# Kernel tuning notes

Measured on AMD Instinct MI355X. Metric: run time of the kernel, lower is better.

The kernel has to match this reference:

```python
import jax, jax.numpy as jnp
import numpy as np

N_NODES = 500_000
N_EDGES = 16_000_000


def setup_inputs() -> dict:
    key = jax.random.key(0)
    ks = jax.random.split(key, 10)
    x = jax.random.normal(ks[0], (N_NODES, 8), dtype=jnp.float32)
    edge_index = jax.random.randint(ks[1], (2, N_EDGES), 0, N_NODES, dtype=jnp.int64)
    W1_l = jax.random.normal(ks[2], (8, 32), dtype=jnp.float32) * 0.1
    W1_r = jax.random.normal(ks[3], (8, 32), dtype=jnp.float32) * 0.1
    b1 = jax.random.normal(ks[4], (32,), dtype=jnp.float32) * 0.1
    W2_l = jax.random.normal(ks[5], (32, 16), dtype=jnp.float32) * 0.1
    W2_r = jax.random.normal(ks[6], (32, 16), dtype=jnp.float32) * 0.1
    b2 = jax.random.normal(ks[7], (16,), dtype=jnp.float32) * 0.1
    W_out = jax.random.normal(ks[8], (16, 1), dtype=jnp.float32) * 0.1
    b_out = jax.random.normal(ks[9], (1,), dtype=jnp.float32) * 0.1
    return {"x": x, "edge_index": edge_index, "W1_l": W1_l, "W1_r": W1_r, "b1": b1,
            "W2_l": W2_l, "W2_r": W2_r, "b2": b2, "W_out": W_out, "b_out": b_out}


def _sage_conv(x, src, dst, deg_inv, W_l, W_r, b):
    # mean-aggregate neighbor features: gather x[src], scatter-add to dst, divide by degree
    agg = jax.ops.segment_sum(x[src], dst, num_segments=N_NODES)  # [N, d_in]
    mean_nb = agg * deg_inv[:, None]
    return mean_nb @ W_l + x @ W_r + b


def reference(x, edge_index, W1_l, W1_r, b1, W2_l, W2_r, b2, W_out, b_out):
    src, dst = edge_index[0], edge_index[1]
    # in-degree per target node (mean aggregation denominator), clamped at 1
    deg = jax.ops.segment_sum(jnp.ones((src.shape[0],), dtype=x.dtype), dst,
                              num_segments=N_NODES)
    deg_inv = 1.0 / jnp.maximum(deg, 1.0)
    h = jax.nn.relu(_sage_conv(x, src, dst, deg_inv, W1_l, W1_r, b1))
    # dropout(p=0.1) is identity at inference
    h = jax.nn.relu(_sage_conv(h, src, dst, deg_inv, W2_l, W2_r, b2))
    return jax.nn.sigmoid(h @ W_out + b_out)  # [N, 1]
```

## Files before the change

kernel.cpp:

```cpp
#include <hip/hip_runtime.h>
#include <hip/hip_fp16.h>
#include <math.h>

#define N_NODES 500000
#define N_EDGES 16000000

#define NBUCKET 2048
#define NPB 256
#define NSB 64
#define NSLICE 32
#define NB_USED 1954
#define BUCKET_CAP 9216

#define NCH_H 500
#define CHUNK_H 32000
#define NCH_A 1000
#define CHUNK_A 16000

#define OFF_TOT     0
#define OFF_BASE    8192
#define OFF_FCUR    16512
#define OFF_SBCUR   24704
#define OFF_AUXB    24960
#define OFF_ROW     25600
#define OFF_DEG     2025600
#define OFF_XH8     4025600
#define OFF_PAIRS   8025664
#define OFF_AUX     72025664
#define OFF_H1P8    72025664
#define OFF_S2      80025664
#define OFF_DEGQ    96025664

typedef float v2f __attribute__((ext_vector_type(2)));
typedef unsigned int v4u __attribute__((ext_vector_type(4)));

static __device__ inline float2 up2(unsigned int u) {
  __half2 h = *reinterpret_cast<__half2*>(&u);
  return __half22float2(h);
}
static __device__ inline unsigned int ph2(float a, float b) {
  __half2 h = __floats2half2_rn(a, b);
  return *reinterpret_cast<unsigned int*>(&h);
}
static __device__ inline unsigned int pk_fp8x4(float a, float b, float c, float d) {
  int u = __builtin_amdgcn_cvt_pk_fp8_f32(a, b, 0, false);
  u = __builtin_amdgcn_cvt_pk_fp8_f32(c, d, u, true);
  return (unsigned int)u;
}
static __device__ inline void acc8(float* a, uint2 g) {
  v2f f01 = __builtin_amdgcn_cvt_pk_f32_fp8((int)g.x, false);
  v2f f23 = __builtin_amdgcn_cvt_pk_f32_fp8((int)g.x, true);
  v2f f45 = __builtin_amdgcn_cvt_pk_f32_fp8((int)g.y, false);
  v2f f67 = __builtin_amdgcn_cvt_pk_f32_fp8((int)g.y, true);
  a[0] += f01.x; a[1] += f01.y; a[2] += f23.x; a[3] += f23.y;
  a[4] += f45.x; a[5] += f45.y; a[6] += f67.x; a[7] += f67.y;
}
static __device__ inline void acc16(float* a, uint4 g) {
  v2f f0 = __builtin_amdgcn_cvt_pk_f32_fp8((int)g.x, false);
  v2f f1 = __builtin_amdgcn_cvt_pk_f32_fp8((int)g.x, true);
  v2f f2 = __builtin_amdgcn_cvt_pk_f32_fp8((int)g.y, false);
  v2f f3 = __builtin_amdgcn_cvt_pk_f32_fp8((int)g.y, true);
  v2f f4 = __builtin_amdgcn_cvt_pk_f32_fp8((int)g.z, false);
  v2f f5 = __builtin_amdgcn_cvt_pk_f32_fp8((int)g.z, true);
  v2f f6 = __builtin_amdgcn_cvt_pk_f32_fp8((int)g.w, false);
  v2f f7 = __builtin_amdgcn_cvt_pk_f32_fp8((int)g.w, true);
  a[0] += f0.x;  a[1] += f0.y;  a[2] += f1.x;  a[3] += f1.y;
  a[4] += f2.x;  a[5] += f2.y;  a[6] += f3.x;  a[7] += f3.y;
  a[8] += f4.x;  a[9] += f4.y;  a[10] += f5.x; a[11] += f5.y;
  a[12] += f6.x; a[13] += f6.y; a[14] += f7.x; a[15] += f7.y;
}

__global__ __launch_bounds__(256) void k_xcast(const float* __restrict__ x,
                                               uint2* __restrict__ xh8) {
  int i = blockIdx.x * 256 + threadIdx.x;
  if (i >= N_NODES) return;
  const float4* xp = (const float4*)(x + (size_t)i * 8);
  float4 a = xp[0], b = xp[1];
  uint2 v;
  v.x = pk_fp8x4(a.x, a.y, a.z, a.w);
  v.y = pk_fp8x4(b.x, b.y, b.z, b.w);
  xh8[i] = v;
}

__global__ __launch_bounds__(256) void k_hist(const int* __restrict__ ei,
                                              int* __restrict__ tot) {
  __shared__ int hist[NBUCKET];
  int t = threadIdx.x;
  int c = blockIdx.x;
#pragma unroll
  for (int j = 0; j < NBUCKET / 256; j++) hist[t + j * 256] = 0;
  __syncthreads();
  int e0 = c * CHUNK_H;
  const int ng = CHUNK_H / 4;
  for (int g = t; g < ng; g += 256) {
    uint4 d4 = *(const uint4*)(ei + N_EDGES + e0 + g * 4);
    atomicAdd(&hist[d4.x >> 8], 1);
    atomicAdd(&hist[d4.y >> 8], 1);
    atomicAdd(&hist[d4.z >> 8], 1);
    atomicAdd(&hist[d4.w >> 8], 1);
  }
  __syncthreads();
#pragma unroll
  for (int j = 0; j < NBUCKET / 256; j++) {
    int b = t + j * 256;
    if (hist[b]) atomicAdd(&tot[b], hist[b]);
  }
}

__global__ __launch_bounds__(256) void k_scan(const int* __restrict__ tot,
                                              int* __restrict__ base,
                                              int* __restrict__ fineCur,
                                              int* __restrict__ sbCur,
                                              int* __restrict__ auxBase) {
  __shared__ int lds[256];
  int t = threadIdx.x;
  int loc[8];
  int s = 0;
#pragma unroll
  for (int j = 0; j < 8; j++) {
    loc[j] = s;
    s += tot[t * 8 + j];
  }
  lds[t] = s;
  __syncthreads();
  for (int off = 1; off < 256; off <<= 1) {
    int v = (t >= off) ? lds[t - off] : 0;
    __syncthreads();
    lds[t] += v;
    __syncthreads();
  }
  int eb = (t > 0) ? lds[t - 1] : 0;
#pragma unroll
  for (int j = 0; j < 8; j++) {
    int idx = t * 8 + j;
    int v = eb + loc[j];
    base[idx] = v;
    fineCur[idx] = v;
  }
  if (t == 255) base[NBUCKET] = lds[255];
  if (t < NSB) {
    int v = (t > 0) ? lds[t * 4 - 1] : 0;
    if (t >= 32) v -= lds[127];
    sbCur[t] = v;
    auxBase[t] = v;
  }
}

__global__ __launch_bounds__(256) void k_passA(const int* __restrict__ ei,
                                               int* __restrict__ sbCur,
                                               unsigned int* __restrict__ aux,
                                               int half) {
  __shared__ int hist[NSB];
  __shared__ int cur[NSB];
  int t = threadIdx.x;
  int c = blockIdx.x;
  if (t < NSB) hist[t] = 0;
  __syncthreads();
  int e0 = c * CHUNK_A;
  const int ng = CHUNK_A / 4;
  for (int g = t; g < ng; g += 256) {
    uint4 d4 = *(const uint4*)(ei + N_EDGES + e0 + g * 4);
    unsigned int dd[4] = {d4.x, d4.y, d4.z, d4.w};
#pragma unroll
    for (int j = 0; j < 4; j++) {
      int sb = (int)(dd[j] >> 13);
      if ((sb >> 5) == half) atomicAdd(&hist[sb], 1);
    }
  }
  __syncthreads();
  if (t < NSB) cur[t] = atomicAdd(&sbCur[t], hist[t]);
  __syncthreads();
  for (int g = t; g < ng; g += 256) {
    uint4 s4 = *(const uint4*)(ei + e0 + g * 4);
    uint4 d4 = *(const uint4*)(ei + N_EDGES + e0 + g * 4);
    unsigned int ss[4] = {s4.x, s4.y, s4.z, s4.w};
    unsigned int dd[4] = {d4.x, d4.y, d4.z, d4.w};
#pragma unroll
    for (int j = 0; j < 4; j++) {
      int sb = (int)(dd[j] >> 13);
      if ((sb >> 5) == half) {
        int pos = atomicAdd(&cur[sb], 1);
        aux[pos] = ss[j] | ((dd[j] & 8191u) << 19);
      }
    }
  }
}

__global__ __launch_bounds__(256) void k_passB(const unsigned int* __restrict__ aux,
                                               const int* __restrict__ base,
                                               const int* __restrict__ auxBase,
                                               int* __restrict__ fineCur,
                                               unsigned int* __restrict__ pairs,
                                               int half) {
  __shared__ int hist[32];
  __shared__ int cur[32];
  int t = threadIdx.x;
  int sbl = blockIdx.x / NSLICE;
  int sl = blockIdx.x % NSLICE;
  int sb = half * 32 + sbl;
  int aStart = auxBase[sb];
  int len = base[(sb + 1) << 5] - base[sb << 5];
  int per = (len + NSLICE - 1) / NSLICE;
  int lo = sl * per;
  int hi = lo + per;
  if (hi > len) hi = len;
  if (t < 32) hist[t] = 0;
  __syncthreads();
  for (int k = lo + t; k < hi; k += 256) {
    unsigned int w = aux[aStart + k];
    atomicAdd(&hist[w >> 27], 1);
  }
  __syncthreads();
  if (t < 32) cur[t] = atomicAdd(&fineCur[(sb << 5) + t], hist[t]);
  __syncthreads();
  for (int k = lo + t; k < hi; k += 256) {
    unsigned int w = aux[aStart + k];
    int pos = atomicAdd(&cur[w >> 27], 1);
    pairs[pos] = w;
  }
}

__global__ __launch_bounds__(256) void k_sort(unsigned int* __restrict__ pairs,
                                              const int* __restrict__ base,
                                              int* __restrict__ row,
                                              int* __restrict__ deg,
                                              unsigned int* __restrict__ degq) {
  __shared__ unsigned int sp[BUCKET_CAP];
  __shared__ int hist[1024];
  __shared__ int cur[1024];
  __shared__ int lds[256];
  int t = threadIdx.x;
  int b = blockIdx.x;
  int e0 = base[b];
  int n = base[b + 1] - e0;
  if (n > BUCKET_CAP) n = BUCKET_CAP;
  for (int k = t; k < n; k += 256) sp[k] = pairs[e0 + k];
#pragma unroll
  for (int j = 0; j < 4; j++) hist[t + j * 256] = 0;
  __syncthreads();
  for (int k = t; k < n; k += 256) {
    unsigned int p = sp[k];
    int key = (int)(((p >> 19) & 255u) << 2) | (int)((p & 0x7FFFFu) >> 17);
    atomicAdd(&hist[key], 1);
  }
  __syncthreads();
  int h0 = hist[4 * t], h1 = hist[4 * t + 1], h2 = hist[4 * t + 2], h3 = hist[4 * t + 3];
  int s = h0 + h1 + h2 + h3;
  lds[t] = s;
  __syncthreads();
  for (int off = 1; off < 256; off <<= 1) {
    int v = (t >= off) ? lds[t - off] : 0;
    __syncthreads();
    lds[t] += v;
    __syncthreads();
  }
  int ebase = (t > 0) ? lds[t - 1] : 0;
  cur[4 * t] = e0 + ebase;
  cur[4 * t + 1] = e0 + ebase + h0;
  cur[4 * t + 2] = e0 + ebase + h0 + h1;
  cur[4 * t + 3] = e0 + ebase + h0 + h1 + h2;
  int i = (b << 8) + t;
  if (i < N_NODES) {
    row[i] = e0 + ebase;
    deg[i] = s;
    degq[i] = (unsigned)h0 | ((unsigned)h1 << 8) | ((unsigned)h2 << 16) |
              ((unsigned)h3 << 24);
  }
  __syncthreads();
  for (int k = t; k < n; k += 256) {
    unsigned int p = sp[k];
    int key = (int)(((p >> 19) & 255u) << 2) | (int)((p & 0x7FFFFu) >> 17);
    int pos = atomicAdd(&cur[key], 1);
    pairs[pos] = p & 0x7FFFFu;
  }
}

__global__ __launch_bounds__(256) void k_l1(
    const unsigned int* __restrict__ adj, const int* __restrict__ row,
    const unsigned int* __restrict__ degq, const uint2* __restrict__ xh8,
    const float* __restrict__ x,
    const float* __restrict__ W1l, const float* __restrict__ W1r,
    const float* __restrict__ b1,
    const float* __restrict__ W2l, const float* __restrict__ W2r,
    v4u* __restrict__ h1p8, v4u* __restrict__ s2) {
  __shared__ float sW1l[256], sW1r[256], sb1[32], sW2l[512], sW2r[512];
  int t = threadIdx.x;
  sW1l[t] = W1l[t];
  sW1r[t] = W1r[t];
  sW2l[t] = W2l[t];  sW2l[t + 256] = W2l[t + 256];
  sW2r[t] = W2r[t];  sW2r[t + 256] = W2r[t + 256];
  if (t < 32) sb1[t] = b1[t];
  __syncthreads();

  int i = blockIdx.x * 256 + t;
  if (i >= N_NODES) return;
  int rs = row[i];
  unsigned dq = degq[i];
  int d = (int)((dq & 255u) + ((dq >> 8) & 255u) + ((dq >> 16) & 255u) + (dq >> 24));

  float acc[8] = {0, 0, 0, 0, 0, 0, 0, 0};
  int off = 0;
#pragma unroll
  for (int q = 0; q < 4; q++) {
    int len = (int)((dq >> (8 * q)) & 255u);
    int js = rs + off;
    int j = 0;
    for (; j + 4 <= len; j += 4) {
      int a0 = (int)__builtin_nontemporal_load(&adj[js + j + 0]);
      int a1 = (int)__builtin_nontemporal_load(&adj[js + j + 1]);
      int a2 = (int)__builtin_nontemporal_load(&adj[js + j + 2]);
      int a3 = (int)__builtin_nontemporal_load(&adj[js + j + 3]);
      uint2 g0 = xh8[a0], g1 = xh8[a1], g2 = xh8[a2], g3 = xh8[a3];
      acc8(acc, g0); acc8(acc, g1); acc8(acc, g2); acc8(acc, g3);
    }
    for (; j < len; j++) {
      uint2 g = xh8[(int)__builtin_nontemporal_load(&adj[js + j])];
      acc8(acc, g);
    }
    off += len;
  }

  float dinv = 1.0f / fmaxf((float)d, 1.0f);
  float m[8];
#pragma unroll
  for (int f = 0; f < 8; f++) m[f] = acc[f] * dinv;
  const float4* xp = (const float4*)(x + (size_t)i * 8);
  float4 x0 = xp[0], x1 = xp[1];
  float xv[8] = {x0.x, x0.y, x0.z, x0.w, x1.x, x1.y, x1.z, x1.w};

  float h[32];
#pragma unroll
  for (int jj = 0; jj < 32; jj++) h[jj] = sb1[jj];
#pragma unroll
  for (int k = 0; k < 8; k++) {
#pragma unroll
    for (int jj = 0; jj < 32; jj++) {
      h[jj] = fmaf(m[k], sW1l[k * 32 + jj], h[jj]);
      h[jj] = fmaf(xv[k], sW1r[k * 32 + jj], h[jj]);
    }
  }
#pragma unroll
  for (int jj = 0; jj < 32; jj++) h[jj] = fmaxf(h[jj], 0.0f);

  float p[16], s[16];
#pragma unroll
  for (int jj = 0; jj < 16; jj++) { p[jj] = 0.0f; s[jj] = 0.0f; }
#pragma unroll
  for (int k = 0; k < 32; k++) {
#pragma unroll
    for (int jj = 0; jj < 16; jj++) {
      p[jj] = fmaf(h[k], sW2l[k * 16 + jj], p[jj]);
      s[jj] = fmaf(h[k], sW2r[k * 16 + jj], s[jj]);
    }
  }
  v4u hv;
  hv.x = pk_fp8x4(p[0], p[1], p[2], p[3]);
  hv.y = pk_fp8x4(p[4], p[5], p[6], p[7]);
  hv.z = pk_fp8x4(p[8], p[9], p[10], p[11]);
  hv.w = pk_fp8x4(p[12], p[13], p[14], p[15]);
  __builtin_nontemporal_store(hv, &h1p8[i]);
  v4u slo, shi;
  slo.x = ph2(s[0], s[1]);   slo.y = ph2(s[2], s[3]);
  slo.z = ph2(s[4], s[5]);   slo.w = ph2(s[6], s[7]);
  shi.x = ph2(s[8], s[9]);   shi.y = ph2(s[10], s[11]);
  shi.z = ph2(s[12], s[13]); shi.w = ph2(s[14], s[15]);
  __builtin_nontemporal_store(slo, &s2[(size_t)i * 2]);
  __builtin_nontemporal_store(shi, &s2[(size_t)i * 2 + 1]);
}

__global__ __launch_bounds__(256) void k_l2(
    const unsigned int* __restrict__ adj, const int* __restrict__ row,
    const unsigned int* __restrict__ degq, const uint4* __restrict__ h1p8,
    const v4u* __restrict__ s2, const float* __restrict__ b2,
    const float* __restrict__ Wout, const float* __restrict__ bout,
    float* __restrict__ out) {
  __shared__ float sb2[16], sWo[16], sbo;
  int t = threadIdx.x;
  if (t < 16) { sb2[t] = b2[t]; sWo[t] = Wout[t]; }
  if (t == 0) sbo = bout[0];
  __syncthreads();

  int i = blockIdx.x * 256 + t;
  if (i >= N_NODES) return;
  int rs = row[i];
  unsigned dq = degq[i];
  int d = (int)((dq & 255u) + ((dq >> 8) & 255u) + ((dq >> 16) & 255u) + (dq >> 24));

  float acc[16];
#pragma unroll
  for (int jj = 0; jj < 16; jj++) acc[jj] = 0.0f;
  int off = 0;
#pragma unroll
  for (int q = 0; q < 4; q++) {
    int len = (int)((dq >> (8 * q)) & 255u);
    int js = rs + off;
    int j = 0;
    for (; j + 4 <= len; j += 4) {
      int a0 = (int)__builtin_nontemporal_load(&adj[js + j + 0]);
      int a1 = (int)__builtin_nontemporal_load(&adj[js + j + 1]);
      int a2 = (int)__builtin_nontemporal_load(&adj[js + j + 2]);
      int a3 = (int)__builtin_nontemporal_load(&adj[js + j + 3]);
      uint4 g0 = h1p8[a0], g1 = h1p8[a1], g2 = h1p8[a2], g3 = h1p8[a3];
      acc16(acc, g0); acc16(acc, g1); acc16(acc, g2); acc16(acc, g3);
    }
    for (; j < len; j++) {
      uint4 g = h1p8[(int)__builtin_nontemporal_load(&adj[js + j])];
      acc16(acc, g);
    }
    off += len;
  }

  float dinv = 1.0f / fmaxf((float)d, 1.0f);
  v4u q0 = __builtin_nontemporal_load(&s2[(size_t)i * 2]);
  v4u q1 = __builtin_nontemporal_load(&s2[(size_t)i * 2 + 1]);
  float2 s0 = up2(q0.x), s1 = up2(q0.y), s2v = up2(q0.z), s3 = up2(q0.w);
  float2 s4 = up2(q1.x), s5 = up2(q1.y), s6 = up2(q1.z), s7 = up2(q1.w);
  float sv[16] = {s0.x, s0.y, s1.x, s1.y, s2v.x, s2v.y, s3.x, s3.y,
                  s4.x, s4.y, s5.x, s5.y, s6.x, s6.y, s7.x, s7.y};
  float o = sbo;
#pragma unroll
  for (int c = 0; c < 16; c++) {
    float h2 = fmaxf(acc[c] * dinv + sv[c] + sb2[c], 0.0f);
    o = fmaf(h2, sWo[c], o);
  }
  out[i] = 1.0f / (1.0f + expf(-o));
}

extern "C" void kernel_launch(void* const* d_in, const int* in_sizes, int n_in,
                              void* d_out, int out_size, void* d_ws, size_t ws_size,
                              hipStream_t stream) {
  const float* x    = (const float*)d_in[0];
  const int*   ei   = (const int*)d_in[1];
  const float* W1l  = (const float*)d_in[2];
  const float* W1r  = (const float*)d_in[3];
  const float* b1   = (const float*)d_in[4];
  const float* W2l  = (const float*)d_in[5];
  const float* W2r  = (const float*)d_in[6];
  const float* b2   = (const float*)d_in[7];
  const float* Wout = (const float*)d_in[8];
  const float* bout = (const float*)d_in[9];
  float* out = (float*)d_out;

  char* ws = (char*)d_ws;
  int* tot     = (int*)(ws + OFF_TOT);
  int* base    = (int*)(ws + OFF_BASE);
  int* fineCur = (int*)(ws + OFF_FCUR);
  int* sbCur   = (int*)(ws + OFF_SBCUR);
  int* auxBase = (int*)(ws + OFF_AUXB);
  int* row     = (int*)(ws + OFF_ROW);
  int* deg     = (int*)(ws + OFF_DEG);
  uint2* xh8   = (uint2*)(ws + OFF_XH8);
  unsigned int* pairs = (unsigned int*)(ws + OFF_PAIRS);
  unsigned int* aux   = (unsigned int*)(ws + OFF_AUX);
  v4u* h1p8    = (v4u*)(ws + OFF_H1P8);
  v4u* s2      = (v4u*)(ws + OFF_S2);
  unsigned int* degq = (unsigned int*)(ws + OFF_DEGQ);

  (void)hipMemsetAsync(tot, 0, NBUCKET * sizeof(int), stream);

  k_xcast<<<NB_USED, 256, 0, stream>>>(x, xh8);
  k_hist<<<NCH_H, 256, 0, stream>>>(ei, tot);
  k_scan<<<1, 256, 0, stream>>>(tot, base, fineCur, sbCur, auxBase);
  k_passA<<<NCH_A, 256, 0, stream>>>(ei, sbCur, aux, 0);
  k_passB<<<32 * NSLICE, 256, 0, stream>>>(aux, base, auxBase, fineCur, pairs, 0);
  k_passA<<<NCH_A, 256, 0, stream>>>(ei, sbCur, aux, 1);
  k_passB<<<32 * NSLICE, 256, 0, stream>>>(aux, base, auxBase, fineCur, pairs, 1);
  k_sort<<<NBUCKET, 256, 0, stream>>>(pairs, base, row, deg, degq);
  k_l1<<<NB_USED, 256, 0, stream>>>(pairs, row, degq, xh8, x, W1l, W1r, b1,
                                    W2l, W2r, h1p8, s2);
  k_l2<<<NB_USED, 256, 0, stream>>>(pairs, row, degq, (const uint4*)h1p8, s2,
                                    b2, Wout, bout, out);
}
```

Measured before the change: 880.8 us.

## Stage radix scatter in LDS per tile for coalesced writes; simplify l1 degree loop

The two scatter passes (passA, passB) now bucket each 4000-element tile in shared memory using per-tile histograms and precomputed global bases. They then write contiguous runs per bucket to global memory with nontemporal stores, where before each element was a scattered direct write. The goal is to cut uncoalesced global write traffic in the multi-pass bucket sort, at the cost of extra LDS traffic, more barriers and a serial per-tile prefix done by one thread. Separately, k_l1 reads the plain degree and loops once over the neighbours instead of four quarter-segments decoded from the packed degq.

```diff
diff --git a/kernel.cpp b/kernel.cpp
--- a/kernel.cpp
+++ b/kernel.cpp
@@ -16,6 +16,8 @@
 #define CHUNK_H 32000
 #define NCH_A 1000
 #define CHUNK_A 16000
+#define T_A 4000
+#define T_B 4000
 
 #define OFF_TOT     0
 #define OFF_BASE    8192
@@ -150,39 +152,76 @@
                                                int* __restrict__ sbCur,
                                                unsigned int* __restrict__ aux,
                                                int half) {
-  __shared__ int hist[NSB];
-  __shared__ int cur[NSB];
+  __shared__ unsigned int ldsW[T_A];
+  __shared__ unsigned char sid[T_A];
+  __shared__ int hist[4 * 32];
+  __shared__ int gbase[4 * 32];
+  __shared__ int loff[32];
+  __shared__ int lcur[32];
+  __shared__ int tot_s;
   int t = threadIdx.x;
   int c = blockIdx.x;
-  if (t < NSB) hist[t] = 0;
-  __syncthreads();
   int e0 = c * CHUNK_A;
-  const int ng = CHUNK_A / 4;
-  for (int g = t; g < ng; g += 256) {
-    uint4 d4 = *(const uint4*)(ei + N_EDGES + e0 + g * 4);
-    unsigned int dd[4] = {d4.x, d4.y, d4.z, d4.w};
-#pragma unroll
-    for (int j = 0; j < 4; j++) {
-      int sb = (int)(dd[j] >> 13);
-      if ((sb >> 5) == half) atomicAdd(&hist[sb], 1);
-    }
-  }
-  __syncthreads();
-  if (t < NSB) cur[t] = atomicAdd(&sbCur[t], hist[t]);
-  __syncthreads();
-  for (int g = t; g < ng; g += 256) {
-    uint4 s4 = *(const uint4*)(ei + e0 + g * 4);
-    uint4 d4 = *(const uint4*)(ei + N_EDGES + e0 + g * 4);
-    unsigned int ss[4] = {s4.x, s4.y, s4.z, s4.w};
-    unsigned int dd[4] = {d4.x, d4.y, d4.z, d4.w};
-#pragma unroll
-    for (int j = 0; j < 4; j++) {
-      int sb = (int)(dd[j] >> 13);
-      if ((sb >> 5) == half) {
-        int pos = atomicAdd(&cur[sb], 1);
-        aux[pos] = ss[j] | ((dd[j] & 8191u) << 19);
+  int sb0 = half * 32;
+  if (t < 128) hist[t] = 0;
+  __syncthreads();
+  {
+    const int ng = CHUNK_A / 4;
+    for (int g = t; g < ng; g += 256) {
+      uint4 d4 = *(const uint4*)(ei + N_EDGES + e0 + g * 4);
+      int tile = g / (T_A / 4);
+      unsigned dd[4] = {d4.x, d4.y, d4.z, d4.w};
+#pragma unroll
+      for (int j = 0; j < 4; j++) {
+        int sb = (int)(dd[j] >> 13);
+        if ((sb >> 5) == half) atomicAdd(&hist[tile * 32 + (sb - sb0)], 1);
       }
     }
+  }
+  __syncthreads();
+  if (t < 32) {
+    int h0 = hist[t], h1 = hist[32 + t], h2 = hist[64 + t], h3 = hist[96 + t];
+    int g = atomicAdd(&sbCur[sb0 + t], h0 + h1 + h2 + h3);
+    gbase[t] = g;
+    gbase[32 + t] = g + h0;
+    gbase[64 + t] = g + h0 + h1;
+    gbase[96 + t] = g + h0 + h1 + h2;
+  }
+  __syncthreads();
+  for (int ti = 0; ti < 4; ti++) {
+    if (t == 0) {
+      int r = 0;
+      for (int s = 0; s < 32; s++) {
+        loff[s] = r; lcur[s] = r; r += hist[ti * 32 + s];
+      }
+      tot_s = r;
+    }
+    __syncthreads();
+    int tb = e0 + ti * T_A;
+    const int ng = T_A / 4;
+    for (int g = t; g < ng; g += 256) {
+      uint4 s4 = *(const uint4*)(ei + tb + g * 4);
+      uint4 d4 = *(const uint4*)(ei + N_EDGES + tb + g * 4);
+      unsigned ss[4] = {s4.x, s4.y, s4.z, s4.w};
+      unsigned dd[4] = {d4.x, d4.y, d4.z, d4.w};
+#pragma unroll
+      for (int j = 0; j < 4; j++) {
+        int sb = (int)(dd[j] >> 13);
+        if ((sb >> 5) == half) {
+          int sl = sb - sb0;
+          int pos = atomicAdd(&lcur[sl], 1);
+          ldsW[pos] = ss[j] | ((dd[j] & 8191u) << 19);
+          sid[pos] = (unsigned char)sl;
+        }
+      }
+    }
+    __syncthreads();
+    int tot = tot_s;
+    for (int k = t; k < tot; k += 256) {
+      int s = sid[k];
+      __builtin_nontemporal_store(ldsW[k], &aux[gbase[ti * 32 + s] + (k - loff[s])]);
+    }
+    __syncthreads();
   }
 }
 
@@ -192,8 +231,13 @@
                                                int* __restrict__ fineCur,
                                                unsigned int* __restrict__ pairs,
                                                int half) {
-  __shared__ int hist[32];
-  __shared__ int cur[32];
+  __shared__ unsigned int ldsW[T_B];
+  __shared__ unsigned char sid[T_B];
+  __shared__ int hist[4 * 32];
+  __shared__ int gbase[4 * 32];
+  __shared__ int loff[32];
+  __shared__ int lcur[32];
+  __shared__ int tot_s;
   int t = threadIdx.x;
   int sbl = blockIdx.x / NSLICE;
   int sl = blockIdx.x % NSLICE;
@@ -204,19 +248,51 @@
   int lo = sl * per;
   int hi = lo + per;
   if (hi > len) hi = len;
-  if (t < 32) hist[t] = 0;
+  if (lo >= hi) return;
+  int nt = (hi - lo + T_B - 1) / T_B;
+  if (t < 128) hist[t] = 0;
   __syncthreads();
   for (int k = lo + t; k < hi; k += 256) {
-    unsigned int w = aux[aStart + k];
-    atomicAdd(&hist[w >> 27], 1);
-  }
-  __syncthreads();
-  if (t < 32) cur[t] = atomicAdd(&fineCur[(sb << 5) + t], hist[t]);
-  __syncthreads();
-  for (int k = lo + t; k < hi; k += 256) {
-    unsigned int w = aux[aStart + k];
-    int pos = atomicAdd(&cur[w >> 27], 1);
-    pairs[pos] = w;
+    unsigned w = aux[aStart + k];
+    int tile = (k - lo) / T_B;
+    atomicAdd(&hist[tile * 32 + (int)(w >> 27)], 1);
+  }
+  __syncthreads();
+  if (t < 32) {
+    int h0 = hist[t], h1 = hist[32 + t], h2 = hist[64 + t], h3 = hist[96 + t];
+    int g = atomicAdd(&fineCur[(sb << 5) + t], h0 + h1 + h2 + h3);
+    gbase[t] = g;
+    gbase[32 + t] = g + h0;
+    gbase[64 + t] = g + h0 + h1;
+    gbase[96 + t] = g + h0 + h1 + h2;
+  }
+  __syncthreads();
+  for (int ti = 0; ti < nt; ti++) {
+    if (t == 0) {
+      int r = 0;
+      for (int s = 0; s < 32; s++) {
+        loff[s] = r; lcur[s] = r; r += hist[ti * 32 + s];
+      }
+      tot_s = r;
+    }
+    __syncthreads();
+    int tl = lo + ti * T_B;
+    int te = tl + T_B;
+    if (te > hi) te = hi;
+    for (int k = tl + t; k < te; k += 256) {
+      unsigned w = aux[aStart + k];
+      int s = (int)(w >> 27);
+      int pos = atomicAdd(&lcur[s], 1);
+      ldsW[pos] = w;
+      sid[pos] = (unsigned char)s;
+    }
+    __syncthreads();
+    int tot = tot_s;
+    for (int k = t; k < tot; k += 256) {
+      int s = sid[k];
+      __builtin_nontemporal_store(ldsW[k], &pairs[gbase[ti * 32 + s] + (k - loff[s])]);
+    }
+    __syncthreads();
   }
 }
 
@@ -277,7 +353,7 @@
 
 __global__ __launch_bounds__(256) void k_l1(
     const unsigned int* __restrict__ adj, const int* __restrict__ row,
-    const unsigned int* __restrict__ degq, const uint2* __restrict__ xh8,
+    const int* __restrict__ deg, const uint2* __restrict__ xh8,
     const float* __restrict__ x,
     const float* __restrict__ W1l, const float* __restrict__ W1r,
     const float* __restrict__ b1,
@@ -295,29 +371,21 @@
   int i = blockIdx.x * 256 + t;
   if (i >= N_NODES) return;
   int rs = row[i];
-  unsigned dq = degq[i];
-  int d = (int)((dq & 255u) + ((dq >> 8) & 255u) + ((dq >> 16) & 255u) + (dq >> 24));
+  int d = deg[i];
 
   float acc[8] = {0, 0, 0, 0, 0, 0, 0, 0};
-  int off = 0;
-#pragma unroll
-  for (int q = 0; q < 4; q++) {
-    int len = (int)((dq >> (8 * q)) & 255u);
-    int js = rs + off;
-    int j = 0;
-    for (; j + 4 <= len; j += 4) {
-      int a0 = (int)__builtin_nontemporal_load(&adj[js + j + 0]);
-      int a1 = (int)__builtin_nontemporal_load(&adj[js + j + 1]);
-      int a2 = (int)__builtin_nontemporal_load(&adj[js + j + 2]);
-      int a3 = (int)__builtin_nontemporal_load(&adj[js + j + 3]);
-      uint2 g0 = xh8[a0], g1 = xh8[a1], g2 = xh8[a2], g3 = xh8[a3];
-      acc8(acc, g0); acc8(acc, g1); acc8(acc, g2); acc8(acc, g3);
-    }
-    for (; j < len; j++) {
-      uint2 g = xh8[(int)__builtin_nontemporal_load(&adj[js + j])];
-      acc8(acc, g);
-    }
-    off += len;
+  int j = 0;
+  for (; j + 4 <= d; j += 4) {
+    int a0 = (int)__builtin_nontemporal_load(&adj[rs + j + 0]);
+    int a1 = (int)__builtin_nontemporal_load(&adj[rs + j + 1]);
+    int a2 = (int)__builtin_nontemporal_load(&adj[rs + j + 2]);
+    int a3 = (int)__builtin_nontemporal_load(&adj[rs + j + 3]);
+    uint2 g0 = xh8[a0], g1 = xh8[a1], g2 = xh8[a2], g3 = xh8[a3];
+    acc8(acc, g0); acc8(acc, g1); acc8(acc, g2); acc8(acc, g3);
+  }
+  for (; j < d; j++) {
+    uint2 g = xh8[(int)__builtin_nontemporal_load(&adj[rs + j])];
+    acc8(acc, g);
   }
 
   float dinv = 1.0f / fmaxf((float)d, 1.0f);
@@ -466,7 +534,7 @@
   k_passA<<<NCH_A, 256, 0, stream>>>(ei, sbCur, aux, 1);
   k_passB<<<32 * NSLICE, 256, 0, stream>>>(aux, base, auxBase, fineCur, pairs, 1);
   k_sort<<<NBUCKET, 256, 0, stream>>>(pairs, base, row, deg, degq);
-  k_l1<<<NB_USED, 256, 0, stream>>>(pairs, row, degq, xh8, x, W1l, W1r, b1,
+  k_l1<<<NB_USED, 256, 0, stream>>>(pairs, row, deg, xh8, x, W1l, W1r, b1,
                                     W2l, W2r, h1p8, s2);
   k_l2<<<NB_USED, 256, 0, stream>>>(pairs, row, degq, (const uint4*)h1p8, s2,
                                     b2, Wout, bout, out);
```

Result: faster. 846.6 us (-3.9%).

## Replace two-level aux scatter with single-pass 2048-bucket scatter

Applied to the files above, without the earlier changes.

Drops the two-half superbucket pass (passA/passB through an aux buffer) in favour of a single scatter kernel that histograms all 2048 fine buckets in LDS and writes directly into the pairs array with nontemporal stores. This removes one full read and write of the 16M-edge intermediate plus four kernel launches, but spreads each block's writes across 2048 destinations instead of 32, so coalescing may suffer. It also simplifies the layer-1 gather loop to one flat loop over the degree, and adds block-wide barriers between quarter passes in layer 2, apparently to keep the threads of a block in lockstep for cache locality.

```diff
diff --git a/kernel.cpp b/kernel.cpp
--- a/kernel.cpp
+++ b/kernel.cpp
@@ -6,27 +6,20 @@
 #define N_EDGES 16000000
 
 #define NBUCKET 2048
-#define NPB 256
-#define NSB 64
-#define NSLICE 32
 #define NB_USED 1954
 #define BUCKET_CAP 9216
 
 #define NCH_H 500
 #define CHUNK_H 32000
-#define NCH_A 1000
-#define CHUNK_A 16000
+#define NCH_S 1000
+#define CHUNK_S 16000
 
 #define OFF_TOT     0
 #define OFF_BASE    8192
 #define OFF_FCUR    16512
-#define OFF_SBCUR   24704
-#define OFF_AUXB    24960
 #define OFF_ROW     25600
-#define OFF_DEG     2025600
 #define OFF_XH8     4025600
 #define OFF_PAIRS   8025664
-#define OFF_AUX     72025664
 #define OFF_H1P8    72025664
 #define OFF_S2      80025664
 #define OFF_DEGQ    96025664
@@ -109,9 +102,7 @@
 
 __global__ __launch_bounds__(256) void k_scan(const int* __restrict__ tot,
                                               int* __restrict__ base,
-                                              int* __restrict__ fineCur,
-                                              int* __restrict__ sbCur,
-                                              int* __restrict__ auxBase) {
+                                              int* __restrict__ fineCur) {
   __shared__ int lds[256];
   int t = threadIdx.x;
   int loc[8];
@@ -138,37 +129,34 @@
     fineCur[idx] = v;
   }
   if (t == 255) base[NBUCKET] = lds[255];
-  if (t < NSB) {
-    int v = (t > 0) ? lds[t * 4 - 1] : 0;
-    if (t >= 32) v -= lds[127];
-    sbCur[t] = v;
-    auxBase[t] = v;
-  }
-}
-
-__global__ __launch_bounds__(256) void k_passA(const int* __restrict__ ei,
-                                               int* __restrict__ sbCur,
-                                               unsigned int* __restrict__ aux,
-                                               int half) {
-  __shared__ int hist[NSB];
-  __shared__ int cur[NSB];
+}
+
+__global__ __launch_bounds__(256) void k_scatter(const int* __restrict__ ei,
+                                                 int* __restrict__ fineCur,
+                                                 unsigned int* __restrict__ pairs) {
+  __shared__ int hist[NBUCKET];
+  __shared__ int cur[NBUCKET];
   int t = threadIdx.x;
   int c = blockIdx.x;
-  if (t < NSB) hist[t] = 0;
-  __syncthreads();
-  int e0 = c * CHUNK_A;
-  const int ng = CHUNK_A / 4;
+  int e0 = c * CHUNK_S;
+#pragma unroll
+  for (int j = 0; j < NBUCKET / 256; j++) hist[t + j * 256] = 0;
+  __syncthreads();
+  const int ng = CHUNK_S / 4;
   for (int g = t; g < ng; g += 256) {
     uint4 d4 = *(const uint4*)(ei + N_EDGES + e0 + g * 4);
-    unsigned int dd[4] = {d4.x, d4.y, d4.z, d4.w};
-#pragma unroll
-    for (int j = 0; j < 4; j++) {
-      int sb = (int)(dd[j] >> 13);
-      if ((sb >> 5) == half) atomicAdd(&hist[sb], 1);
-    }
-  }
-  __syncthreads();
-  if (t < NSB) cur[t] = atomicAdd(&sbCur[t], hist[t]);
+    atomicAdd(&hist[d4.x >> 8], 1);
+    atomicAdd(&hist[d4.y >> 8], 1);
+    atomicAdd(&hist[d4.z >> 8], 1);
+    atomicAdd(&hist[d4.w >> 8], 1);
+  }
+  __syncthreads();
+#pragma unroll
+  for (int j = 0; j < NBUCKET / 256; j++) {
+    int b = t + j * 256;
+    int h = hist[b];
+    cur[b] = h ? atomicAdd(&fineCur[b], h) : 0;
+  }
   __syncthreads();
   for (int g = t; g < ng; g += 256) {
     uint4 s4 = *(const uint4*)(ei + e0 + g * 4);
@@ -177,53 +165,16 @@
     unsigned int dd[4] = {d4.x, d4.y, d4.z, d4.w};
 #pragma unroll
     for (int j = 0; j < 4; j++) {
-      int sb = (int)(dd[j] >> 13);
-      if ((sb >> 5) == half) {
-        int pos = atomicAdd(&cur[sb], 1);
-        aux[pos] = ss[j] | ((dd[j] & 8191u) << 19);
-      }
+      int b = (int)(dd[j] >> 8);
+      int pos = atomicAdd(&cur[b], 1);
+      __builtin_nontemporal_store(ss[j] | ((dd[j] & 255u) << 19), &pairs[pos]);
     }
-  }
-}
-
-__global__ __launch_bounds__(256) void k_passB(const unsigned int* __restrict__ aux,
-                                               const int* __restrict__ base,
-                                               const int* __restrict__ auxBase,
-                                               int* __restrict__ fineCur,
-                                               unsigned int* __restrict__ pairs,
-                                               int half) {
-  __shared__ int hist[32];
-  __shared__ int cur[32];
-  int t = threadIdx.x;
-  int sbl = blockIdx.x / NSLICE;
-  int sl = blockIdx.x % NSLICE;
-  int sb = half * 32 + sbl;
-  int aStart = auxBase[sb];
-  int len = base[(sb + 1) << 5] - base[sb << 5];
-  int per = (len + NSLICE - 1) / NSLICE;
-  int lo = sl * per;
-  int hi = lo + per;
-  if (hi > len) hi = len;
-  if (t < 32) hist[t] = 0;
-  __syncthreads();
-  for (int k = lo + t; k < hi; k += 256) {
-    unsigned int w = aux[aStart + k];
-    atomicAdd(&hist[w >> 27], 1);
-  }
-  __syncthreads();
-  if (t < 32) cur[t] = atomicAdd(&fineCur[(sb << 5) + t], hist[t]);
-  __syncthreads();
-  for (int k = lo + t; k < hi; k += 256) {
-    unsigned int w = aux[aStart + k];
-    int pos = atomicAdd(&cur[w >> 27], 1);
-    pairs[pos] = w;
   }
 }
 
 __global__ __launch_bounds__(256) void k_sort(unsigned int* __restrict__ pairs,
                                               const int* __restrict__ base,
                                               int* __restrict__ row,
-                                              int* __restrict__ deg,
                                               unsigned int* __restrict__ degq) {
   __shared__ unsigned int sp[BUCKET_CAP];
   __shared__ int hist[1024];
@@ -262,7 +213,6 @@
   int i = (b << 8) + t;
   if (i < N_NODES) {
     row[i] = e0 + ebase;
-    deg[i] = s;
     degq[i] = (unsigned)h0 | ((unsigned)h1 << 8) | ((unsigned)h2 << 16) |
               ((unsigned)h3 << 24);
   }
@@ -299,25 +249,18 @@
   int d = (int)((dq & 255u) + ((dq >> 8) & 255u) + ((dq >> 16) & 255u) + (dq >> 24));
 
   float acc[8] = {0, 0, 0, 0, 0, 0, 0, 0};
-  int off = 0;
-#pragma unroll
-  for (int q = 0; q < 4; q++) {
-    int len = (int)((dq >> (8 * q)) & 255u);
-    int js = rs + off;
-    int j = 0;
-    for (; j + 4 <= len; j += 4) {
-      int a0 = (int)__builtin_nontemporal_load(&adj[js + j + 0]);
-      int a1 = (int)__builtin_nontemporal_load(&adj[js + j + 1]);
-      int a2 = (int)__builtin_nontemporal_load(&adj[js + j + 2]);
-      int a3 = (int)__builtin_nontemporal_load(&adj[js + j + 3]);
-      uint2 g0 = xh8[a0], g1 = xh8[a1], g2 = xh8[a2], g3 = xh8[a3];
-      acc8(acc, g0); acc8(acc, g1); acc8(acc, g2); acc8(acc, g3);
-    }
-    for (; j < len; j++) {
-      uint2 g = xh8[(int)__builtin_nontemporal_load(&adj[js + j])];
-      acc8(acc, g);
-    }
-    off += len;
+  int j = 0;
+  for (; j + 4 <= d; j += 4) {
+    int a0 = (int)__builtin_nontemporal_load(&adj[rs + j + 0]);
+    int a1 = (int)__builtin_nontemporal_load(&adj[rs + j + 1]);
+    int a2 = (int)__builtin_nontemporal_load(&adj[rs + j + 2]);
+    int a3 = (int)__builtin_nontemporal_load(&adj[rs + j + 3]);
+    uint2 g0 = xh8[a0], g1 = xh8[a1], g2 = xh8[a2], g3 = xh8[a3];
+    acc8(acc, g0); acc8(acc, g1); acc8(acc, g2); acc8(acc, g3);
+  }
+  for (; j < d; j++) {
+    uint2 g = xh8[(int)__builtin_nontemporal_load(&adj[rs + j])];
+    acc8(acc, g);
   }
 
   float dinv = 1.0f / fmaxf((float)d, 1.0f);
@@ -381,9 +324,9 @@
   __syncthreads();
 
   int i = blockIdx.x * 256 + t;
-  if (i >= N_NODES) return;
-  int rs = row[i];
-  unsigned dq = degq[i];
+  bool act = i < N_NODES;
+  int rs = act ? row[i] : 0;
+  unsigned dq = act ? degq[i] : 0;
   int d = (int)((dq & 255u) + ((dq >> 8) & 255u) + ((dq >> 16) & 255u) + (dq >> 24));
 
   float acc[16];
@@ -408,8 +351,10 @@
       acc16(acc, g);
     }
     off += len;
-  }
-
+    if (q < 3) __syncthreads();
+  }
+
+  if (!act) return;
   float dinv = 1.0f / fmaxf((float)d, 1.0f);
   v4u q0 = __builtin_nontemporal_load(&s2[(size_t)i * 2]);
   v4u q1 = __builtin_nontemporal_load(&s2[(size_t)i * 2 + 1]);
@@ -445,13 +390,9 @@
   int* tot     = (int*)(ws + OFF_TOT);
   int* base    = (int*)(ws + OFF_BASE);
   int* fineCur = (int*)(ws + OFF_FCUR);
-  int* sbCur   = (int*)(ws + OFF_SBCUR);
-  int* auxBase = (int*)(ws + OFF_AUXB);
   int* row     = (int*)(ws + OFF_ROW);
-  int* deg     = (int*)(ws + OFF_DEG);
   uint2* xh8   = (uint2*)(ws + OFF_XH8);
   unsigned int* pairs = (unsigned int*)(ws + OFF_PAIRS);
-  unsigned int* aux   = (unsigned int*)(ws + OFF_AUX);
   v4u* h1p8    = (v4u*)(ws + OFF_H1P8);
   v4u* s2      = (v4u*)(ws + OFF_S2);
   unsigned int* degq = (unsigned int*)(ws + OFF_DEGQ);
@@ -460,12 +401,9 @@
 
   k_xcast<<<NB_USED, 256, 0, stream>>>(x, xh8);
   k_hist<<<NCH_H, 256, 0, stream>>>(ei, tot);
-  k_scan<<<1, 256, 0, stream>>>(tot, base, fineCur, sbCur, auxBase);
-  k_passA<<<NCH_A, 256, 0, stream>>>(ei, sbCur, aux, 0);
-  k_passB<<<32 * NSLICE, 256, 0, stream>>>(aux, base, auxBase, fineCur, pairs, 0);
-  k_passA<<<NCH_A, 256, 0, stream>>>(ei, sbCur, aux, 1);
-  k_passB<<<32 * NSLICE, 256, 0, stream>>>(aux, base, auxBase, fineCur, pairs, 1);
-  k_sort<<<NBUCKET, 256, 0, stream>>>(pairs, base, row, deg, degq);
+  k_scan<<<1, 256, 0, stream>>>(tot, base, fineCur);
+  k_scatter<<<NCH_S, 256, 0, stream>>>(ei, fineCur, pairs);
+  k_sort<<<NBUCKET, 256, 0, stream>>>(pairs, base, row, degq);
   k_l1<<<NB_USED, 256, 0, stream>>>(pairs, row, degq, xh8, x, W1l, W1r, b1,
                                     W2l, W2r, h1p8, s2);
   k_l2<<<NB_USED, 256, 0, stream>>>(pairs, row, degq, (const uint4*)h1p8, s2,
```

New measurement: 1.358 ms. 54.2% more time.
